# Kernel optimization log

Measured on AMD Instinct MI355X. Metric: run time of the kernel, lower is better.

The kernel has to match this reference:

```python
import jax, jax.numpy as jnp
import numpy as np
from jax import lax

BETA = 0.5          # module default beta
WD_ITERATION = 50   # module default wd_iteration
ERR_TOL = 0.1       # early-exit threshold in IPOT loop
EPS_FILL = 1e-8     # masked_fill value


def setup_inputs() -> dict:
    key = jax.random.key(0)
    k1, k2 = jax.random.split(key)
    bs, N = 128, 512
    # non-negative cost matrix, bs x N x N
    C = jax.random.uniform(k1, (bs, N, N), dtype=jnp.float32)
    # boolean node mask, bs x N; guarantee at least one valid node per graph
    mask = jax.random.uniform(k2, (bs, N)) < 0.8
    mask = mask.at[:, 0].set(True)
    return {"C": C, "bs": bs, "N_s": N, "N_t": N, "mask": mask}


def _ipot_T(C, mask, beta=BETA, iteration=WD_ITERATION):
    m = mask.astype(jnp.float32)                                   # (bs, N)
    mu = (m / jnp.sum(m, axis=1, keepdims=True))[:, :, None]       # (bs, N, 1)
    mv = mu
    T0 = m[:, :, None] * m[:, None, :]                             # bmm(mask, mask^T)
    A = jnp.exp(-C / beta)
    notmask = ~mask[:, :, None]                                    # (bs, N, 1)

    def step(carry, _):
        T, sigma, done = carry
        Q = A * T
        b = jnp.einsum('bnm,bmk->bnk', Q, sigma)                   # Q @ sigma
        b = jnp.where(notmask, EPS_FILL, b)
        delta = mu / b
        a = jnp.einsum('bnm,bnk->bmk', Q, delta)                   # Q^T @ delta
        a = jnp.where(notmask, EPS_FILL, a)
        sigma_new = mv / a
        T_new = delta * Q * jnp.swapaxes(sigma_new, 1, 2)
        err = jnp.max(jnp.sum(jnp.abs(T_new - T), axis=-1))        # global max, as in torch
        # emulate host-side early exit: once converged, freeze state
        T_out = jnp.where(done, T, T_new)
        sigma_out = jnp.where(done, sigma, sigma_new)
        done_out = done | (err < ERR_TOL)
        return (T_out, sigma_out, done_out), None

    (T, _, _), _ = lax.scan(step, (T0, mu, jnp.array(False)), None, length=iteration)
    return T


def reference(C, bs, N_s, N_t, mask):
    T = _ipot_T(C, mask)
    distance = jnp.sum(T * C, axis=(-2, -1))                       # (bs,)
    return (distance, T, C)
```

## Files before the change

### kernel.cpp

```cpp
#include <hip/hip_runtime.h>

#define INVB  2.0f
#define TOL   0.1f
#define EPS   1e-8f
#define NITER 50
#define NP    4


__device__ __forceinline__ float wsum(float v) {
    #pragma unroll
    for (int o = 1; o < 64; o <<= 1) v += __shfl_xor(v, o, 64);
    return v;
}

__device__ __forceinline__ void group_arrive(unsigned* flagp) {
    __hip_atomic_fetch_add(flagp, 1u, __ATOMIC_RELEASE, __HIP_MEMORY_SCOPE_AGENT);
}
__device__ __forceinline__ void group_wait(unsigned* flagp, unsigned target) {
    long sp = 0;
    while (__hip_atomic_load(flagp, __ATOMIC_RELAXED, __HIP_MEMORY_SCOPE_AGENT)
               < target && sp < (1L << 24)) {
        __builtin_amdgcn_s_sleep(2); ++sp;
    }
    (void)__hip_atomic_load(flagp, __ATOMIC_ACQUIRE, __HIP_MEMORY_SCOPE_AGENT);
}

__global__ void k_zero(unsigned* ctrl, int ctrlwords, int* mode,
                       const unsigned* mraw, int nwords) {
    const int t = threadIdx.x;
    for (int i = t; i < ctrlwords; i += 1024) ctrl[i] = 0u;
    __shared__ int sF, sB;
    if (t == 0) { sF = 0; sB = 0; }
    __syncthreads();
    int f = 0, b = 0;
    for (int i = t; i < nwords; i += 1024) {
        unsigned w = mraw[i];
        if (w == 0x3f800000u) f = 1;
        else if (w > 1u)      b = 1;
    }
    if (f) atomicOr(&sF, 1);
    if (b) atomicOr(&sB, 1);
    __syncthreads();
    if (t == 0) *mode = sF ? 2 : (sB ? 1 : 0);
}

__global__ __launch_bounds__(1024, 8) void k_ipot4(
    const float* __restrict__ C, const void* __restrict__ mraw,
    int bs, int N,
    unsigned* err_u, unsigned* flags, float* dpart, const int* mode_p,
    float* apart, float* outD, float* outT, float* outC)
{
    const int g    = blockIdx.x >> 2;
    const int p    = blockIdx.x & 3;
    const int t    = threadIdx.x;
    const int lane = t & 63;
    const int wv   = t >> 6;
    const int NR   = N >> 2;
    const int r0   = p * NR;
    const int rpw  = NR >> 4;
    const float NEG = -__builtin_inff();
    unsigned* flagp = &flags[g * 16];

    __shared__ __align__(16) float ls_s[512];
    __shared__ __align__(16) float lsp_s[512];
    __shared__ __align__(16) float lsig_s[512];
    __shared__ __align__(16) float m01[512];
    __shared__ float ld_own[128], ldp_own[128];
    __shared__ __align__(16) float ap_ws[16][512];
    __shared__ float red_s[16];
    __shared__ float muv_s, lmu_s, errg_s;
    __shared__ unsigned errbits_s;

    {
        const int mode = *mode_p;
        if (t < N) {
            const int idx = g * N + t;
            bool mv;
            if (mode == 1)      mv = ((const unsigned char*)mraw)[idx] != 0;
            else if (mode == 2) mv = ((const float*)mraw)[idx] != 0.0f;
            else                mv = ((const int*)mraw)[idx] != 0;
            m01[t] = mv ? 1.f : 0.f;
            const float z = mv ? 0.f : NEG;
            ls_s[t] = z; lsp_s[t] = z;
        }
        __syncthreads();
        if (t < N) {
            float v = wsum(m01[t]);
            if (lane == 0) red_s[wv] = v;
        }
        __syncthreads();
        if (t == 0) {
            float cnt = 0.f;
            for (int i = 0; i < (N >> 6); ++i) cnt += red_s[i];
            muv_s = 1.0f / cnt;
            lmu_s = __logf(muv_s);
        }
        __syncthreads();
        if (t < N) lsig_s[t] = (m01[t] != 0.f) ? lmu_s : NEG;
        if (t < NR) {
            const float z = (m01[r0 + t] != 0.f) ? 0.f : NEG;
            ld_own[t] = z; ldp_own[t] = z;
        }
        __syncthreads();
    }
    const float muv = muv_s, lmu = lmu_s;
    unsigned rnd = 0;

    {
        float4 fa[2] = {{0,0,0,0},{0,0,0,0}};
        for (int j = 0; j < rpw; ++j) {
            const int lo = wv * rpw + j;
            const int n  = r0 + lo;
            const bool valid = m01[n] != 0.f;
            const float* crow = C + ((size_t)g * N + n) * N;
            float bacc = 0.f;
            if (valid) {
                #pragma unroll
                for (int mg = 0; mg < 2; ++mg) {
                    const int mb = mg * 256 + lane * 4;
                    float4 c4 = *(const float4*)(crow + mb);
                    float4 m4 = *(const float4*)(&m01[mb]);
                    bacc += m4.x * __expf(lmu - INVB * c4.x);
                    bacc += m4.y * __expf(lmu - INVB * c4.y);
                    bacc += m4.z * __expf(lmu - INVB * c4.z);
                    bacc += m4.w * __expf(lmu - INVB * c4.w);
                }
            }
            bacc = wsum(bacc);
            const float ldn1 = valid ? __logf(muv / bacc) : NEG;
            if (lane == 0) ld_own[lo] = ldn1;
            if (valid) {
                #pragma unroll
                for (int mg = 0; mg < 2; ++mg) {
                    const int mb = mg * 256 + lane * 4;
                    float4 c4 = *(const float4*)(crow + mb);
                    float4 l4 = *(const float4*)(&ls_s[mb]);
                    fa[mg].x += __expf(ldn1 + l4.x - INVB * c4.x);
                    fa[mg].y += __expf(ldn1 + l4.y - INVB * c4.y);
                    fa[mg].z += __expf(ldn1 + l4.z - INVB * c4.z);
                    fa[mg].w += __expf(ldn1 + l4.w - INVB * c4.w);
                }
            }
        }
        *(float4*)&ap_ws[wv][lane * 4]       = fa[0];
        *(float4*)&ap_ws[wv][256 + lane * 4] = fa[1];
        __syncthreads();
        if (t < N) {
            float av = 0.f;
            #pragma unroll
            for (int w = 0; w < 16; ++w) av += ap_ws[w][t];
            apart[((size_t)(g * NP + p)) * N + t] = av;
        }
        __syncthreads();
        ++rnd;
        if (t == 0) { group_arrive(flagp); group_wait(flagp, NP * rnd); }
        __syncthreads();
        if (t < N && m01[t] != 0.f) {
            float av = 0.f;
            #pragma unroll
            for (int q = 0; q < NP; ++q) av += apart[((size_t)(g * NP + q)) * N + t];
            const float lsg = __logf(muv / av);
            lsp_s[t] = ls_s[t]; ls_s[t] += lsg; lsig_s[t] = lsg;
        }
        __syncthreads();
    }

    int kf = NITER;
    for (int it = 0; it < NITER; ++it) {
        const float s1 = (float)it * INVB;
        const float s2 = s1 + INVB;
        const float s3 = s2 + INVB;
        if (t == 0) errbits_s = 0u;
        float4 fa[2] = {{0,0,0,0},{0,0,0,0}};
        float errmax = 0.f;
        __syncthreads();

        for (int j = 0; j < rpw; ++j) {
            const int lo = wv * rpw + j;
            const int n  = r0 + lo;
            const bool valid = m01[n] != 0.f;
            const float ldn = ld_own[lo], ldo = ldp_own[lo];
            const float* crow = C + ((size_t)g * N + n) * N;
            float eacc = 0.f, bacc = 0.f;
            if (valid) {
                #pragma unroll
                for (int mg = 0; mg < 2; ++mg) {
                    const int mb = mg * 256 + lane * 4;
                    float4 c4  = *(const float4*)(crow + mb);
                    float4 ln4 = *(const float4*)(&ls_s[mb]);
                    float4 lo4 = *(const float4*)(&lsp_s[mb]);
                    float4 lg4 = *(const float4*)(&lsig_s[mb]);
                    float tn, to;
                    tn = __expf(ldn + ln4.x - s2 * c4.x);
                    to = __expf(ldo + lo4.x - s1 * c4.x);
                    eacc += fabsf(tn - to);
                    bacc += __expf(ldn + ln4.x + lg4.x - s3 * c4.x);
                    tn = __expf(ldn + ln4.y - s2 * c4.y);
                    to = __expf(ldo + lo4.y - s1 * c4.y);
                    eacc += fabsf(tn - to);
                    bacc += __expf(ldn + ln4.y + lg4.y - s3 * c4.y);
                    tn = __expf(ldn + ln4.z - s2 * c4.z);
                    to = __expf(ldo + lo4.z - s1 * c4.z);
                    eacc += fabsf(tn - to);
                    bacc += __expf(ldn + ln4.z + lg4.z - s3 * c4.z);
                    tn = __expf(ldn + ln4.w - s2 * c4.w);
                    to = __expf(ldo + lo4.w - s1 * c4.w);
                    eacc += fabsf(tn - to);
                    bacc += __expf(ldn + ln4.w + lg4.w - s3 * c4.w);
                }
            }
            bacc = wsum(bacc);
            eacc = wsum(eacc);
            errmax = fmaxf(errmax, eacc);
            const float ldn2 = valid ? (ldn + __logf(muv / bacc)) : NEG;
            if (lane == 0) { ldp_own[lo] = ldn; ld_own[lo] = ldn2; }
            if (valid) {
                #pragma unroll
                for (int mg = 0; mg < 2; ++mg) {
                    const int mb = mg * 256 + lane * 4;
                    float4 c4 = *(const float4*)(crow + mb);
                    float4 l4 = *(const float4*)(&ls_s[mb]);
                    fa[mg].x += __expf(ldn2 + l4.x - s3 * c4.x);
                    fa[mg].y += __expf(ldn2 + l4.y - s3 * c4.y);
                    fa[mg].z += __expf(ldn2 + l4.z - s3 * c4.z);
                    fa[mg].w += __expf(ldn2 + l4.w - s3 * c4.w);
                }
            }
        }
        if (lane == 0) atomicMax(&errbits_s, __float_as_uint(errmax));
        *(float4*)&ap_ws[wv][lane * 4]       = fa[0];
        *(float4*)&ap_ws[wv][256 + lane * 4] = fa[1];
        __syncthreads();
        if (t < N) {
            float av = 0.f;
            #pragma unroll
            for (int w = 0; w < 16; ++w) av += ap_ws[w][t];
            apart[((size_t)(g * NP + p)) * N + t] = av;
        }
        if (t == 0) atomicMax(&err_u[g * 64 + it], errbits_s);
        __syncthreads();
        ++rnd;
        if (t == 0) {
            group_arrive(flagp); group_wait(flagp, NP * rnd);
            errg_s = __uint_as_float(err_u[g * 64 + it]);
        }
        __syncthreads();
        if (errg_s < TOL) { kf = it + 1; break; }
        if (it == NITER - 1) { kf = NITER; break; }
        if (t < N && m01[t] != 0.f) {
            float av = 0.f;
            #pragma unroll
            for (int q = 0; q < NP; ++q) av += apart[((size_t)(g * NP + q)) * N + t];
            const float lsg = __logf(muv / av);
            lsp_s[t] = ls_s[t]; ls_s[t] += lsg; lsig_s[t] = lsg;
        }
        __syncthreads();
    }

    float dacc = 0.f;
    {
        const float sF = (float)kf * INVB;
        for (int j = 0; j < rpw; ++j) {
            const int lo = wv * rpw + j;
            const int gr = g * N + r0 + lo;
            const float ldv = ldp_own[lo];
            const float* crow = C + (size_t)gr * N;
            float* trow = outT + (size_t)gr * N;
            float* orow = outC + (size_t)gr * N;
            #pragma unroll
            for (int mg = 0; mg < 2; ++mg) {
                const int mb = mg * 256 + lane * 4;
                float4 c4 = *(const float4*)(crow + mb);
                float4 l4 = *(const float4*)(&ls_s[mb]);
                float4 t4;
                t4.x = __expf(ldv + l4.x - sF * c4.x);
                t4.y = __expf(ldv + l4.y - sF * c4.y);
                t4.z = __expf(ldv + l4.z - sF * c4.z);
                t4.w = __expf(ldv + l4.w - sF * c4.w);
                dacc += t4.x * c4.x + t4.y * c4.y + t4.z * c4.z + t4.w * c4.w;
                *(float4*)(trow + mb) = t4;
                *(float4*)(orow + mb) = c4;
            }
        }
    }
    dacc = wsum(dacc);
    if (lane == 0) red_s[wv] = dacc;
    __syncthreads();
    ++rnd;
    if (t == 0) {
        float d = 0.f;
        #pragma unroll
        for (int w = 0; w < 16; ++w) d += red_s[w];
        dpart[g * NP + p] = d;
        group_arrive(flagp);
        if (p == 0) {
            group_wait(flagp, NP * rnd);
            float dt = 0.f;
            #pragma unroll
            for (int q = 0; q < NP; ++q) dt += dpart[g * NP + q];
            outD[g] = dt;
        }
    }
}

extern "C" void kernel_launch(void* const* d_in, const int* in_sizes, int n_in,
                              void* d_out, int out_size, void* d_ws, size_t ws_size,
                              hipStream_t stream) {
    const float* C    = (const float*)d_in[0];
    const void*  mask = d_in[4];
    const int R  = in_sizes[4];
    const int N  = in_sizes[0] / R;
    const int bs = R / N;

    unsigned* wsu   = (unsigned*)d_ws;
    unsigned* err_u = wsu;
    unsigned* flags = wsu + (size_t)bs * 64;
    float*    dpart = (float*)(flags + (size_t)bs * 16);
    int*      mode  = (int*)(dpart + (size_t)bs * NP);
    const int ctrlwords = bs * 64 + bs * 16 + bs * NP + 1;
    float*    apart = (float*)(wsu + ((ctrlwords + 255) & ~255));

    float* outD = (float*)d_out;
    float* outT = outD + bs;
    float* outC = outT + (size_t)bs * N * N;

    k_zero<<<1, 1024, 0, stream>>>(wsu, ctrlwords, mode,
                                   (const unsigned*)mask, R / 4);
    k_ipot4<<<bs * NP, 1024, 0, stream>>>(C, mask, bs, N,
                                          err_u, flags, dpart, mode,
                                          apart, outD, outT, outC);
}
```

Measured before the change: 236.6 us.

## Cut exp count per element in IPOT loop via factored Sinkhorn terms and prefetch

```diff
diff --git a/kernel.cpp b/kernel.cpp
--- a/kernel.cpp
+++ b/kernel.cpp
@@ -5,6 +5,8 @@
 #define EPS   1e-8f
 #define NITER 50
 #define NP    4
+
+typedef float f32x4 __attribute__((ext_vector_type(4)));
 
 
 __device__ __forceinline__ float wsum(float v) {
@@ -61,14 +63,14 @@
     const float NEG = -__builtin_inff();
     unsigned* flagp = &flags[g * 16];
 
+    __shared__ __align__(16) float m01[512];
     __shared__ __align__(16) float ls_s[512];
-    __shared__ __align__(16) float lsp_s[512];
-    __shared__ __align__(16) float lsig_s[512];
-    __shared__ __align__(16) float m01[512];
-    __shared__ float ld_own[128], ldp_own[128];
+    __shared__ __align__(16) float sig_s[512];
+    __shared__ __align__(16) float rs_s[512];
+    __shared__ float ld_own[128], ldp_own[128], ldr_own[128];
     __shared__ __align__(16) float ap_ws[16][512];
     __shared__ float red_s[16];
-    __shared__ float muv_s, lmu_s, errg_s;
+    __shared__ float muv_s, cnt_s, errg_s;
     __shared__ unsigned errbits_s;
 
     {
@@ -79,9 +81,9 @@
             if (mode == 1)      mv = ((const unsigned char*)mraw)[idx] != 0;
             else if (mode == 2) mv = ((const float*)mraw)[idx] != 0.0f;
             else                mv = ((const int*)mraw)[idx] != 0;
-            m01[t] = mv ? 1.f : 0.f;
-            const float z = mv ? 0.f : NEG;
-            ls_s[t] = z; lsp_s[t] = z;
+            m01[t]  = mv ? 1.f : 0.f;
+            ls_s[t] = mv ? 0.f : NEG;
+            sig_s[t] = 0.f; rs_s[t] = 0.f;
         }
         __syncthreads();
         if (t < N) {
@@ -92,58 +94,145 @@
         if (t == 0) {
             float cnt = 0.f;
             for (int i = 0; i < (N >> 6); ++i) cnt += red_s[i];
+            cnt_s = cnt;
             muv_s = 1.0f / cnt;
-            lmu_s = __logf(muv_s);
-        }
-        __syncthreads();
-        if (t < N) lsig_s[t] = (m01[t] != 0.f) ? lmu_s : NEG;
-        if (t < NR) {
-            const float z = (m01[r0 + t] != 0.f) ? 0.f : NEG;
-            ld_own[t] = z; ldp_own[t] = z;
-        }
-        __syncthreads();
-    }
-    const float muv = muv_s, lmu = lmu_s;
+        }
+        __syncthreads();
+    }
+    const float muv = muv_s, cnt = cnt_s;
     unsigned rnd = 0;
 
+    const float* wbase = C + ((size_t)g * N + r0 + wv * rpw) * N + lane * 4;
+    const int mb0 = lane * 4, mb1 = 256 + lane * 4;
+
     {
-        float4 fa[2] = {{0,0,0,0},{0,0,0,0}};
+        float4 ca = *(const float4*)(wbase);
+        float4 cb = *(const float4*)(wbase + 256);
+        const float4 m40 = *(const float4*)(&m01[mb0]);
+        const float4 m41 = *(const float4*)(&m01[mb1]);
+        float4 fa0 = {0,0,0,0}, fa1 = {0,0,0,0};
         for (int j = 0; j < rpw; ++j) {
+            const int jn = (j + 1 < rpw) ? (j + 1) : j;
+            const float4 na = *(const float4*)(wbase + (size_t)jn * N);
+            const float4 nb = *(const float4*)(wbase + (size_t)jn * N + 256);
             const int lo = wv * rpw + j;
-            const int n  = r0 + lo;
-            const bool valid = m01[n] != 0.f;
-            const float* crow = C + ((size_t)g * N + n) * N;
-            float bacc = 0.f;
-            if (valid) {
-                #pragma unroll
-                for (int mg = 0; mg < 2; ++mg) {
-                    const int mb = mg * 256 + lane * 4;
-                    float4 c4 = *(const float4*)(crow + mb);
-                    float4 m4 = *(const float4*)(&m01[mb]);
-                    bacc += m4.x * __expf(lmu - INVB * c4.x);
-                    bacc += m4.y * __expf(lmu - INVB * c4.y);
-                    bacc += m4.z * __expf(lmu - INVB * c4.z);
-                    bacc += m4.w * __expf(lmu - INVB * c4.w);
+            const bool valid = m01[r0 + lo] != 0.f;
+            float4 bt0, bt1;
+            bt0.x = m40.x * __expf(-INVB * ca.x);
+            bt0.y = m40.y * __expf(-INVB * ca.y);
+            bt0.z = m40.z * __expf(-INVB * ca.z);
+            bt0.w = m40.w * __expf(-INVB * ca.w);
+            bt1.x = m41.x * __expf(-INVB * cb.x);
+            bt1.y = m41.y * __expf(-INVB * cb.y);
+            bt1.z = m41.z * __expf(-INVB * cb.z);
+            bt1.w = m41.w * __expf(-INVB * cb.w);
+            float bacc = bt0.x + bt0.y + bt0.z + bt0.w
+                       + bt1.x + bt1.y + bt1.z + bt1.w;
+            bacc = wsum(bacc);
+            float q, ld1, ldr;
+            if (valid) { q = 1.0f / bacc; ld1 = __logf(q); ldr = bacc; }
+            else       { q = 0.f;         ld1 = NEG;       ldr = 0.f;  }
+            if (lane == 0) {
+                ld_own[lo]  = ld1;
+                ldp_own[lo] = valid ? 0.f : NEG;
+                ldr_own[lo] = ldr;
+            }
+            fa0.x += q * bt0.x; fa0.y += q * bt0.y;
+            fa0.z += q * bt0.z; fa0.w += q * bt0.w;
+            fa1.x += q * bt1.x; fa1.y += q * bt1.y;
+            fa1.z += q * bt1.z; fa1.w += q * bt1.w;
+            ca = na; cb = nb;
+        }
+        *(float4*)&ap_ws[wv][mb0] = fa0;
+        *(float4*)&ap_ws[wv][mb1] = fa1;
+    }
+    __syncthreads();
+    if (t < N) {
+        float av = 0.f;
+        #pragma unroll
+        for (int w = 0; w < 16; ++w) av += ap_ws[w][t];
+        apart[((size_t)(g * NP + p)) * N + t] = av;
+    }
+    __syncthreads();
+    ++rnd;
+    if (t == 0) { group_arrive(flagp); group_wait(flagp, NP * rnd); }
+    __syncthreads();
+    if (t < N && m01[t] != 0.f) {
+        float av = 0.f;
+        #pragma unroll
+        for (int q2 = 0; q2 < NP; ++q2)
+            av += apart[((size_t)(g * NP + q2)) * N + t];
+        const float sg = muv / av;
+        ls_s[t] += __logf(sg);
+        sig_s[t] = sg;
+        rs_s[t]  = av * cnt;
+    }
+    __syncthreads();
+
+    int kf = NITER;
+    for (int it = 0; it < NITER; ++it) {
+        const float s1 = (float)it * INVB;
+        if (t == 0) errbits_s = 0u;
+        __syncthreads();
+        {
+            float4 ca = *(const float4*)(wbase);
+            float4 cb = *(const float4*)(wbase + 256);
+            float4 fa0 = {0,0,0,0}, fa1 = {0,0,0,0};
+            float errmax = 0.f;
+            for (int j = 0; j < rpw; ++j) {
+                const int jn = (j + 1 < rpw) ? (j + 1) : j;
+                const float4 na = *(const float4*)(wbase + (size_t)jn * N);
+                const float4 nb = *(const float4*)(wbase + (size_t)jn * N + 256);
+                const int lo = wv * rpw + j;
+                const bool valid = m01[r0 + lo] != 0.f;
+                const float ldn = ld_own[lo];
+                const float ldr = ldr_own[lo];
+                const float4 ln0 = *(const float4*)(&ls_s[mb0]);
+                const float4 ln1 = *(const float4*)(&ls_s[mb1]);
+                const float4 sg0 = *(const float4*)(&sig_s[mb0]);
+                const float4 sg1 = *(const float4*)(&sig_s[mb1]);
+                const float4 rs0 = *(const float4*)(&rs_s[mb0]);
+                const float4 rs1 = *(const float4*)(&rs_s[mb1]);
+                float eacc = 0.f, bacc = 0.f;
+                float4 bt0, bt1;
+                #define IPOT_E(cc, LN, SG, RS, BT)                          \
+                  { float F  = __expf(-INVB * (cc));                        \
+                    float G  = __expf(ldn + (LN) - s1 * (cc));              \
+                    float tn = G * F;                                       \
+                    float to = G * ldr * (RS);                              \
+                    eacc += fabsf(tn - to);                                 \
+                    (BT) = tn * F * (SG);                                   \
+                    bacc += (BT); }
+                IPOT_E(ca.x, ln0.x, sg0.x, rs0.x, bt0.x)
+                IPOT_E(ca.y, ln0.y, sg0.y, rs0.y, bt0.y)
+                IPOT_E(ca.z, ln0.z, sg0.z, rs0.z, bt0.z)
+                IPOT_E(ca.w, ln0.w, sg0.w, rs0.w, bt0.w)
+                IPOT_E(cb.x, ln1.x, sg1.x, rs1.x, bt1.x)
+                IPOT_E(cb.y, ln1.y, sg1.y, rs1.y, bt1.y)
+                IPOT_E(cb.z, ln1.z, sg1.z, rs1.z, bt1.z)
+                IPOT_E(cb.w, ln1.w, sg1.w, rs1.w, bt1.w)
+                #undef IPOT_E
+                bacc = wsum(bacc);
+                eacc = wsum(eacc);
+                errmax = fmaxf(errmax, eacc);
+                float q, ldn2, ldrn;
+                if (valid) { q = muv / bacc; ldn2 = ldn + __logf(q); ldrn = bacc * cnt; }
+                else       { q = 0.f;        ldn2 = NEG;             ldrn = 0.f;       }
+                if (lane == 0) {
+                    ldp_own[lo] = ldn;
+                    ld_own[lo]  = ldn2;
+                    ldr_own[lo] = ldrn;
                 }
+                fa0.x += q * bt0.x * rs0.x; fa0.y += q * bt0.y * rs0.y;
+                fa0.z += q * bt0.z * rs0.z; fa0.w += q * bt0.w * rs0.w;
+                fa1.x += q * bt1.x * rs1.x; fa1.y += q * bt1.y * rs1.y;
+                fa1.z += q * bt1.z * rs1.z; fa1.w += q * bt1.w * rs1.w;
+                ca = na; cb = nb;
             }
-            bacc = wsum(bacc);
-            const float ldn1 = valid ? __logf(muv / bacc) : NEG;
-            if (lane == 0) ld_own[lo] = ldn1;
-            if (valid) {
-                #pragma unroll
-                for (int mg = 0; mg < 2; ++mg) {
-                    const int mb = mg * 256 + lane * 4;
-                    float4 c4 = *(const float4*)(crow + mb);
-                    float4 l4 = *(const float4*)(&ls_s[mb]);
-                    fa[mg].x += __expf(ldn1 + l4.x - INVB * c4.x);
-                    fa[mg].y += __expf(ldn1 + l4.y - INVB * c4.y);
-                    fa[mg].z += __expf(ldn1 + l4.z - INVB * c4.z);
-                    fa[mg].w += __expf(ldn1 + l4.w - INVB * c4.w);
-                }
-            }
-        }
-        *(float4*)&ap_ws[wv][lane * 4]       = fa[0];
-        *(float4*)&ap_ws[wv][256 + lane * 4] = fa[1];
+            if (lane == 0) atomicMax(&errbits_s, __float_as_uint(errmax));
+            *(float4*)&ap_ws[wv][mb0] = fa0;
+            *(float4*)&ap_ws[wv][mb1] = fa1;
+        }
         __syncthreads();
         if (t < N) {
             float av = 0.f;
@@ -151,92 +240,6 @@
             for (int w = 0; w < 16; ++w) av += ap_ws[w][t];
             apart[((size_t)(g * NP + p)) * N + t] = av;
         }
-        __syncthreads();
-        ++rnd;
-        if (t == 0) { group_arrive(flagp); group_wait(flagp, NP * rnd); }
-        __syncthreads();
-        if (t < N && m01[t] != 0.f) {
-            float av = 0.f;
-            #pragma unroll
-            for (int q = 0; q < NP; ++q) av += apart[((size_t)(g * NP + q)) * N + t];
-            const float lsg = __logf(muv / av);
-            lsp_s[t] = ls_s[t]; ls_s[t] += lsg; lsig_s[t] = lsg;
-        }
-        __syncthreads();
-    }
-
-    int kf = NITER;
-    for (int it = 0; it < NITER; ++it) {
-        const float s1 = (float)it * INVB;
-        const float s2 = s1 + INVB;
-        const float s3 = s2 + INVB;
-        if (t == 0) errbits_s = 0u;
-        float4 fa[2] = {{0,0,0,0},{0,0,0,0}};
-        float errmax = 0.f;
-        __syncthreads();
-
-        for (int j = 0; j < rpw; ++j) {
-            const int lo = wv * rpw + j;
-            const int n  = r0 + lo;
-            const bool valid = m01[n] != 0.f;
-            const float ldn = ld_own[lo], ldo = ldp_own[lo];
-            const float* crow = C + ((size_t)g * N + n) * N;
-            float eacc = 0.f, bacc = 0.f;
-            if (valid) {
-                #pragma unroll
-                for (int mg = 0; mg < 2; ++mg) {
-                    const int mb = mg * 256 + lane * 4;
-                    float4 c4  = *(const float4*)(crow + mb);
-                    float4 ln4 = *(const float4*)(&ls_s[mb]);
-                    float4 lo4 = *(const float4*)(&lsp_s[mb]);
-                    float4 lg4 = *(const float4*)(&lsig_s[mb]);
-                    float tn, to;
-                    tn = __expf(ldn + ln4.x - s2 * c4.x);
-                    to = __expf(ldo + lo4.x - s1 * c4.x);
-                    eacc += fabsf(tn - to);
-                    bacc += __expf(ldn + ln4.x + lg4.x - s3 * c4.x);
-                    tn = __expf(ldn + ln4.y - s2 * c4.y);
-                    to = __expf(ldo + lo4.y - s1 * c4.y);
-                    eacc += fabsf(tn - to);
-                    bacc += __expf(ldn + ln4.y + lg4.y - s3 * c4.y);
-                    tn = __expf(ldn + ln4.z - s2 * c4.z);
-                    to = __expf(ldo + lo4.z - s1 * c4.z);
-                    eacc += fabsf(tn - to);
-                    bacc += __expf(ldn + ln4.z + lg4.z - s3 * c4.z);
-                    tn = __expf(ldn + ln4.w - s2 * c4.w);
-                    to = __expf(ldo + lo4.w - s1 * c4.w);
-                    eacc += fabsf(tn - to);
-                    bacc += __expf(ldn + ln4.w + lg4.w - s3 * c4.w);
-                }
-            }
-            bacc = wsum(bacc);
-            eacc = wsum(eacc);
-            errmax = fmaxf(errmax, eacc);
-            const float ldn2 = valid ? (ldn + __logf(muv / bacc)) : NEG;
-            if (lane == 0) { ldp_own[lo] = ldn; ld_own[lo] = ldn2; }
-            if (valid) {
-                #pragma unroll
-                for (int mg = 0; mg < 2; ++mg) {
-                    const int mb = mg * 256 + lane * 4;
-                    float4 c4 = *(const float4*)(crow + mb);
-                    float4 l4 = *(const float4*)(&ls_s[mb]);
-                    fa[mg].x += __expf(ldn2 + l4.x - s3 * c4.x);
-                    fa[mg].y += __expf(ldn2 + l4.y - s3 * c4.y);
-                    fa[mg].z += __expf(ldn2 + l4.z - s3 * c4.z);
-                    fa[mg].w += __expf(ldn2 + l4.w - s3 * c4.w);
-                }
-            }
-        }
-        if (lane == 0) atomicMax(&errbits_s, __float_as_uint(errmax));
-        *(float4*)&ap_ws[wv][lane * 4]       = fa[0];
-        *(float4*)&ap_ws[wv][256 + lane * 4] = fa[1];
-        __syncthreads();
-        if (t < N) {
-            float av = 0.f;
-            #pragma unroll
-            for (int w = 0; w < 16; ++w) av += ap_ws[w][t];
-            apart[((size_t)(g * NP + p)) * N + t] = av;
-        }
         if (t == 0) atomicMax(&err_u[g * 64 + it], errbits_s);
         __syncthreads();
         ++rnd;
@@ -250,9 +253,12 @@
         if (t < N && m01[t] != 0.f) {
             float av = 0.f;
             #pragma unroll
-            for (int q = 0; q < NP; ++q) av += apart[((size_t)(g * NP + q)) * N + t];
-            const float lsg = __logf(muv / av);
-            lsp_s[t] = ls_s[t]; ls_s[t] += lsg; lsig_s[t] = lsg;
+            for (int q2 = 0; q2 < NP; ++q2)
+                av += apart[((size_t)(g * NP + q2)) * N + t];
+            const float sg = muv / av;
+            ls_s[t] += __logf(sg);
+            sig_s[t] = sg;
+            rs_s[t]  = av * cnt;
         }
         __syncthreads();
     }
@@ -260,27 +266,35 @@
     float dacc = 0.f;
     {
         const float sF = (float)kf * INVB;
+        float4 ca = *(const float4*)(wbase);
+        float4 cb = *(const float4*)(wbase + 256);
         for (int j = 0; j < rpw; ++j) {
+            const int jn = (j + 1 < rpw) ? (j + 1) : j;
+            const float4 na = *(const float4*)(wbase + (size_t)jn * N);
+            const float4 nb = *(const float4*)(wbase + (size_t)jn * N + 256);
             const int lo = wv * rpw + j;
             const int gr = g * N + r0 + lo;
             const float ldv = ldp_own[lo];
-            const float* crow = C + (size_t)gr * N;
-            float* trow = outT + (size_t)gr * N;
-            float* orow = outC + (size_t)gr * N;
-            #pragma unroll
-            for (int mg = 0; mg < 2; ++mg) {
-                const int mb = mg * 256 + lane * 4;
-                float4 c4 = *(const float4*)(crow + mb);
-                float4 l4 = *(const float4*)(&ls_s[mb]);
-                float4 t4;
-                t4.x = __expf(ldv + l4.x - sF * c4.x);
-                t4.y = __expf(ldv + l4.y - sF * c4.y);
-                t4.z = __expf(ldv + l4.z - sF * c4.z);
-                t4.w = __expf(ldv + l4.w - sF * c4.w);
-                dacc += t4.x * c4.x + t4.y * c4.y + t4.z * c4.z + t4.w * c4.w;
-                *(float4*)(trow + mb) = t4;
-                *(float4*)(orow + mb) = c4;
-            }
+            const float4 ln0 = *(const float4*)(&ls_s[mb0]);
+            const float4 ln1 = *(const float4*)(&ls_s[mb1]);
+            f32x4 t0, t1;
+            t0.x = __expf(ldv + ln0.x - sF * ca.x);
+            t0.y = __expf(ldv + ln0.y - sF * ca.y);
+            t0.z = __expf(ldv + ln0.z - sF * ca.z);
+            t0.w = __expf(ldv + ln0.w - sF * ca.w);
+            t1.x = __expf(ldv + ln1.x - sF * cb.x);
+            t1.y = __expf(ldv + ln1.y - sF * cb.y);
+            t1.z = __expf(ldv + ln1.z - sF * cb.z);
+            t1.w = __expf(ldv + ln1.w - sF * cb.w);
+            dacc += t0.x * ca.x + t0.y * ca.y + t0.z * ca.z + t0.w * ca.w;
+            dacc += t1.x * cb.x + t1.y * cb.y + t1.z * cb.z + t1.w * cb.w;
+            f32x4 c0 = { ca.x, ca.y, ca.z, ca.w };
+            f32x4 c1 = { cb.x, cb.y, cb.z, cb.w };
+            __builtin_nontemporal_store(t0, (f32x4*)(outT + (size_t)gr * N + mb0));
+            __builtin_nontemporal_store(t1, (f32x4*)(outT + (size_t)gr * N + mb1));
+            __builtin_nontemporal_store(c0, (f32x4*)(outC + (size_t)gr * N + mb0));
+            __builtin_nontemporal_store(c1, (f32x4*)(outC + (size_t)gr * N + mb1));
+            ca = na; cb = nb;
         }
     }
     dacc = wsum(dacc);
@@ -297,7 +311,7 @@
             group_wait(flagp, NP * rnd);
             float dt = 0.f;
             #pragma unroll
-            for (int q = 0; q < NP; ++q) dt += dpart[g * NP + q];
+            for (int q2 = 0; q2 < NP; ++q2) dt += dpart[g * NP + q2];
             outD[g] = dt;
         }
     }
```

New measurement: 258.3 us. +9.2%, slower.
